# Kernel optimization log

Measured on AMD Instinct MI355X. Metric: run time of the kernel, lower is better.

Reference implementation:

```python
import jax, jax.numpy as jnp
import numpy as np
from math import factorial, sqrt

# ---- config: irreps_in1 = 128x0e+128x1o+128x2e, irreps_in2 = 1x0e+1x1o+1x2e, out = in1
MUL1, MUL2 = 128, 1
LS = [0, 1, 2]
DIMS = [2 * l + 1 for l in LS]
OFF1 = np.cumsum([0] + [MUL1 * d for d in DIMS])  # block offsets in x1 / out
OFF2 = np.cumsum([0] + [MUL2 * d for d in DIMS])  # block offsets in x2
# (i_in1, i_in2, i_out), all mode 'uvu', has_weight=True, path_weight=1
INSTR = [(0,0,0),(0,1,1),(0,2,2),(1,0,1),(1,1,0),(1,1,2),(1,2,1),(2,0,2),(2,1,1),(2,2,0),(2,2,2)]


def su2_cg(j1, m1, j2, m2, j3, m3):
    # SU(2) Clebsch-Gordan coefficient <j1 m1 j2 m2 | j3 m3> (e3nn convention)
    if m3 != m1 + m2:
        return 0.0
    f = factorial
    vmin = max(-j1 + j2 + m3, -j1 + m1, 0)
    vmax = min(j2 + j3 + m1, j3 - j1 + j2, j3 + m3)
    C = sqrt((2 * j3 + 1) * f(j3 + j1 - j2) * f(j3 - j1 + j2) * f(j1 + j2 - j3)
             * f(j3 + m3) * f(j3 - m3)
             / (f(j1 + j2 + j3 + 1) * f(j1 - m1) * f(j1 + m1) * f(j2 - m2) * f(j2 + m2)))
    S = 0.0
    for v in range(vmin, vmax + 1):
        S += (-1) ** (v + j2 + m2) * f(j2 + j3 + m1 - v) * f(j1 - m1 + v) \
             / (f(v) * f(j3 - j1 + j2 - v) * f(j3 + m3 - v) * f(v + j1 - j2 - m3))
    return C * S


def q_real_to_complex(l):
    # change of basis real SH -> complex SH (e3nn convention incl. (-i)^l phase)
    q = np.zeros((2 * l + 1, 2 * l + 1), dtype=np.complex128)
    for m in range(-l, 0):
        q[l + m, l + abs(m)] = 1 / sqrt(2)
        q[l + m, l - abs(m)] = -1j / sqrt(2)
    q[l, l] = 1.0
    for m in range(1, l + 1):
        q[l + m, l + abs(m)] = (-1) ** m / sqrt(2)
        q[l + m, l - abs(m)] = 1j * (-1) ** m / sqrt(2)
    return (-1j) ** l * q


def wigner_3j(l1, l2, l3):
    # real-basis Wigner 3j (e3nn), Frobenius-normalized
    C = np.zeros((2 * l1 + 1, 2 * l2 + 1, 2 * l3 + 1))
    for m1 in range(-l1, l1 + 1):
        for m2 in range(-l2, l2 + 1):
            for m3 in range(-l3, l3 + 1):
                C[l1 + m1, l2 + m2, l3 + m3] = su2_cg(l1, m1, l2, m2, l3, m3)
    Q1, Q2, Q3 = q_real_to_complex(l1), q_real_to_complex(l2), q_real_to_complex(l3)
    C = np.einsum('ij,kl,mn,ikn->jlm', Q1, Q2, np.conj(Q3.T), C.astype(np.complex128))
    C = np.real(C)
    return (C / np.linalg.norm(C)).astype(np.float32)


_N_PATHS_TO = np.zeros(len(LS), dtype=np.int64)
for _i1, _i2, _io in INSTR:
    _N_PATHS_TO[_io] += 1  # num_elements(uvu)=mul2=1, vars=1 -> element norm divisor


def setup_inputs() -> dict:
    key = jax.random.key(0)
    k1, k2, k3 = jax.random.split(key, 3)
    Z = 50000
    return {
        'x1': jax.random.normal(k1, (Z, int(OFF1[-1])), dtype=jnp.float32),
        'x2': jax.random.normal(k2, (Z, int(OFF2[-1])), dtype=jnp.float32),
        'weight': jax.random.normal(k3, (len(INSTR) * MUL1 * MUL2,), dtype=jnp.float32),
    }


def reference(x1, x2, weight):
    Z = x1.shape[0]
    outs = [jnp.zeros((Z, MUL1, DIMS[i]), x1.dtype) for i in range(len(LS))]
    woff = 0
    for (i1, i2, io) in INSTR:
        d1, d2, do = DIMS[i1], DIMS[i2], DIMS[io]
        x1b = x1[:, OFF1[i1]:OFF1[i1 + 1]].reshape(Z, MUL1, d1)
        x2b = x2[:, OFF2[i2]:OFF2[i2 + 1]].reshape(Z, MUL2, d2)
        w = weight[woff:woff + MUL1 * MUL2].reshape(MUL1, MUL2)
        woff += MUL1 * MUL2
        cg = jnp.asarray(wigner_3j(LS[i1], LS[i2], LS[io]))
        alpha = sqrt(do / float(_N_PATHS_TO[io]))  # component/element normalization
        outs[io] = outs[io] + alpha * jnp.einsum('ijk,uv,zui,zvj->zuk', cg, w, x1b, x2b)
    return jnp.concatenate([o.reshape(Z, -1) for o in outs], axis=1)
```

## Files before the change

### kernel.cpp

```cpp
#include <hip/hip_runtime.h>
#include <cmath>
#include <complex>
#include <algorithm>


namespace {

constexpr int NPATH = 11;
constexpr int P_I1[NPATH] = {0,0,0,1,1,1,1,2,2,2,2};
constexpr int P_I2[NPATH] = {0,1,2,0,1,1,2,0,1,2,2};
constexpr int P_IO[NPATH] = {0,1,2,1,0,2,1,2,1,0,2};
constexpr int DIM_[3]  = {1,3,5};
constexpr int LOFF[3]  = {0,1,4};
constexpr int P_OFF[NPATH] = {0,1,10,35,44,53,98,143,168,213,238};
constexpr int CG_TOTAL = 363;
constexpr int ROWF = 1152;
constexpr int ROWV = ROWF / 4;

typedef float v4f __attribute__((ext_vector_type(4)));

struct CGPack { float c[CG_TOTAL]; };


double fct(int n){ double r = 1.0; for(int i = 2; i <= n; ++i) r *= i; return r; }

double su2_cg(int j1,int m1,int j2,int m2,int j3,int m3){
  if (m3 != m1 + m2) return 0.0;
  int vmin = std::max(std::max(-j1 + j2 + m3, -j1 + m1), 0);
  int vmax = std::min(std::min(j2 + j3 + m1, j3 - j1 + j2), j3 + m3);
  double C = std::sqrt((2.0*j3 + 1.0) * fct(j3 + j1 - j2) * fct(j3 - j1 + j2) * fct(j1 + j2 - j3)
                       * fct(j3 + m3) * fct(j3 - m3)
                       / (fct(j1 + j2 + j3 + 1) * fct(j1 - m1) * fct(j1 + m1)
                          * fct(j2 - m2) * fct(j2 + m2)));
  double S = 0.0;
  for (int v = vmin; v <= vmax; ++v){
    double t = fct(j2 + j3 + m1 - v) * fct(j1 - m1 + v)
             / (fct(v) * fct(j3 - j1 + j2 - v) * fct(j3 + m3 - v) * fct(v + j1 - j2 - m3));
    S += (((v + j2 + m2) & 1) ? -1.0 : 1.0) * t;
  }
  return C * S;
}

void q_mat(int l, std::complex<double> q[5][5]){
  for (int a = 0; a < 5; ++a) for (int b = 0; b < 5; ++b) q[a][b] = 0.0;
  const double s = 1.0 / std::sqrt(2.0);
  for (int m = -l; m < 0; ++m){
    q[l+m][l-m] = s;
    q[l+m][l+m] = std::complex<double>(0.0, -s);
  }
  q[l][l] = 1.0;
  for (int m = 1; m <= l; ++m){
    double sg = (m & 1) ? -1.0 : 1.0;
    q[l+m][l+m] = sg * s;
    q[l+m][l-m] = std::complex<double>(0.0, sg * s);
  }
  std::complex<double> ph(1.0, 0.0);
  const std::complex<double> mi(0.0, -1.0);
  for (int t = 0; t < l; ++t) ph *= mi;
  for (int a = 0; a < 5; ++a) for (int b = 0; b < 5; ++b) q[a][b] *= ph;
}

void wigner3j(int l1, int l2, int l3, double scale, float* dst){
  const int n1 = 2*l1+1, n2 = 2*l2+1, n3 = 2*l3+1;
  std::complex<double> C[5][5][5];
  for (int a = 0; a < 5; ++a) for (int b = 0; b < 5; ++b) for (int c = 0; c < 5; ++c)
    C[a][b][c] = 0.0;
  for (int m1 = -l1; m1 <= l1; ++m1)
    for (int m2 = -l2; m2 <= l2; ++m2)
      for (int m3 = -l3; m3 <= l3; ++m3)
        C[l1+m1][l2+m2][l3+m3] = su2_cg(l1, m1, l2, m2, l3, m3);
  std::complex<double> Q1[5][5], Q2[5][5], Q3[5][5];
  q_mat(l1, Q1); q_mat(l2, Q2); q_mat(l3, Q3);
  double R[5][5][5];
  double nrm = 0.0;
  for (int a = 0; a < n1; ++a)
    for (int b = 0; b < n2; ++b)
      for (int c = 0; c < n3; ++c){
        std::complex<double> s(0.0, 0.0);
        for (int i = 0; i < n1; ++i)
          for (int k = 0; k < n2; ++k)
            for (int n = 0; n < n3; ++n)
              s += Q1[i][a] * Q2[k][b] * std::conj(Q3[n][c]) * C[i][k][n];
        R[a][b][c] = s.real();
        nrm += s.real() * s.real();
      }
  nrm = std::sqrt(nrm);
  for (int a = 0; a < n1; ++a)
    for (int b = 0; b < n2; ++b)
      for (int c = 0; c < n3; ++c)
        dst[(a*n2 + b)*n3 + c] = (float)(scale * R[a][b][c] / nrm);
}

CGPack build_pack(){
  CGPack p;
  int npaths_to[3] = {0,0,0};
  for (int i = 0; i < NPATH; ++i) npaths_to[P_IO[i]]++;
  for (int i = 0; i < NPATH; ++i){
    double alpha = std::sqrt((double)DIM_[P_IO[i]] / (double)npaths_to[P_IO[i]]);
    wigner3j(P_I1[i], P_I2[i], P_IO[i], alpha, p.c + P_OFF[i]);
  }
  return p;
}

}


__global__ __launch_bounds__(256) void tp_uvu_kernel(
    const float* __restrict__ x1, const float* __restrict__ x2,
    const float* __restrict__ w, float* __restrict__ out,
    int Z, CGPack cg)
{
  const int tid  = threadIdx.x;
  const int u    = tid & 127;
  const int zloc = tid >> 7;
  const long zbase = (long)blockIdx.x * 2;
  const long z     = zbase + zloc;

  __shared__ float s_x1[2 * ROWF];
  __shared__ float s_o [2 * ROWF];
  __shared__ float s_x2[2][9];

  const int nvalid_v = (int)((Z - zbase >= 2 ? 2 : (Z - zbase)) * ROWV);
  {
    const v4f* g1 = (const v4f*)(x1 + zbase * ROWF);
    v4f* s1 = (v4f*)s_x1;
    #pragma unroll
    for (int it = 0; it < 3; ++it) {
      int i = tid + it * 256;
      if (i < nvalid_v) s1[i] = g1[i];
    }
  }
  if (z < Z && u < 9) s_x2[zloc][u] = x2[z * 9 + u];
  __syncthreads();

  const float* x1z = s_x1 + zloc * ROWF;
  float xv2[9];
  #pragma unroll
  for (int j = 0; j < 9; ++j) xv2[j] = s_x2[zloc][j];

  float in1[9];
  in1[0] = x1z[u];
  #pragma unroll
  for (int i = 0; i < 3; ++i) in1[1+i] = x1z[128 + u*3 + i];
  #pragma unroll
  for (int i = 0; i < 5; ++i) in1[4+i] = x1z[512 + u*5 + i];

  float o[9];
  #pragma unroll
  for (int k = 0; k < 9; ++k) o[k] = 0.0f;

  #pragma unroll
  for (int p = 0; p < NPATH; ++p){
    const float wv = w[p * 128 + u];
    const int l1 = P_I1[p], l2 = P_I2[p], lo = P_IO[p];
    const int d1 = DIM_[l1], d2 = DIM_[l2], dd = DIM_[lo];
    const int b1 = LOFF[l1], b2 = LOFF[l2], bo = LOFF[lo];
    #pragma unroll
    for (int i = 0; i < d1; ++i){
      #pragma unroll
      for (int j = 0; j < d2; ++j){
        const float t = wv * in1[b1 + i] * xv2[b2 + j];
        #pragma unroll
        for (int k = 0; k < dd; ++k)
          o[bo + k] = fmaf(t, cg.c[P_OFF[p] + (i*d2 + j)*dd + k], o[bo + k]);
      }
    }
  }

  {
    float* oz = s_o + zloc * ROWF;
    oz[u] = o[0];
    #pragma unroll
    for (int k = 0; k < 3; ++k) oz[128 + u*3 + k] = o[1+k];
    #pragma unroll
    for (int k = 0; k < 5; ++k) oz[512 + u*5 + k] = o[4+k];
  }
  __syncthreads();
  {
    v4f* g_o = (v4f*)(out + zbase * ROWF);
    const v4f* s1 = (const v4f*)s_o;
    #pragma unroll
    for (int it = 0; it < 3; ++it) {
      int i = tid + it * 256;
      if (i < nvalid_v) __builtin_nontemporal_store(s1[i], &g_o[i]);
    }
  }
}

extern "C" void kernel_launch(void* const* d_in, const int* in_sizes, int n_in,
                              void* d_out, int out_size, void* d_ws, size_t ws_size,
                              hipStream_t stream)
{
  const float* x1 = (const float*)d_in[0];
  const float* x2 = (const float*)d_in[1];
  const float* w  = (const float*)d_in[2];
  float* out = (float*)d_out;
  const int Z = in_sizes[0] / ROWF;

  CGPack pack = build_pack();

  const int zpb = 2;
  dim3 grid((Z + zpb - 1) / zpb), block(128 * zpb);
  hipLaunchKernelGGL(tp_uvu_kernel, grid, block, 0, stream,
                     x1, x2, w, out, Z, pack);
}
```

Baseline: 396.3 us.

## Compute CG coefficients at compile time and skip zero terms in kernel

Moves the Wigner-3j/Clebsch-Gordan table construction into constexpr evaluation, so the coefficients become compile-time constants inside the kernel instead of a by-value kernel argument. With known values, the unrolled path loop can drop FMAs whose coefficient is zero, which removes most of the dense 363-term work. The per-path weight loads are also hoisted ahead of the compute loop. The risks are small numerical differences from the constexpr sqrt and the near-zero clamping. Host-side table building and the large kernel argument are removed as well.

```diff
diff --git a/kernel.cpp b/kernel.cpp
--- a/kernel.cpp
+++ b/kernel.cpp
@@ -1,6 +1,4 @@
 #include <hip/hip_runtime.h>
-#include <cmath>
-#include <complex>
 #include <algorithm>
 
 
@@ -22,85 +20,106 @@
 struct CGPack { float c[CG_TOTAL]; };
 
 
-double fct(int n){ double r = 1.0; for(int i = 2; i <= n; ++i) r *= i; return r; }
-
-double su2_cg(int j1,int m1,int j2,int m2,int j3,int m3){
+constexpr double cfct(int n){ double r = 1.0; for (int i = 2; i <= n; ++i) r *= i; return r; }
+
+constexpr double csqrt(double x){
+  if (x <= 0.0) return 0.0;
+  double g = x > 1.0 ? x : 1.0;
+  for (int i = 0; i < 64; ++i) g = 0.5 * (g + x / g);
+  return g;
+}
+
+struct cplx { double re = 0.0, im = 0.0; };
+constexpr cplx cmul(cplx a, cplx b){ return {a.re*b.re - a.im*b.im, a.re*b.im + a.im*b.re}; }
+constexpr cplx cconj(cplx a){ return {a.re, -a.im}; }
+
+constexpr double su2_cg(int j1,int m1,int j2,int m2,int j3,int m3){
   if (m3 != m1 + m2) return 0.0;
   int vmin = std::max(std::max(-j1 + j2 + m3, -j1 + m1), 0);
   int vmax = std::min(std::min(j2 + j3 + m1, j3 - j1 + j2), j3 + m3);
-  double C = std::sqrt((2.0*j3 + 1.0) * fct(j3 + j1 - j2) * fct(j3 - j1 + j2) * fct(j1 + j2 - j3)
-                       * fct(j3 + m3) * fct(j3 - m3)
-                       / (fct(j1 + j2 + j3 + 1) * fct(j1 - m1) * fct(j1 + m1)
-                          * fct(j2 - m2) * fct(j2 + m2)));
+  double C = csqrt((2.0*j3 + 1.0) * cfct(j3 + j1 - j2) * cfct(j3 - j1 + j2) * cfct(j1 + j2 - j3)
+                   * cfct(j3 + m3) * cfct(j3 - m3)
+                   / (cfct(j1 + j2 + j3 + 1) * cfct(j1 - m1) * cfct(j1 + m1)
+                      * cfct(j2 - m2) * cfct(j2 + m2)));
   double S = 0.0;
   for (int v = vmin; v <= vmax; ++v){
-    double t = fct(j2 + j3 + m1 - v) * fct(j1 - m1 + v)
-             / (fct(v) * fct(j3 - j1 + j2 - v) * fct(j3 + m3 - v) * fct(v + j1 - j2 - m3));
+    double t = cfct(j2 + j3 + m1 - v) * cfct(j1 - m1 + v)
+             / (cfct(v) * cfct(j3 - j1 + j2 - v) * cfct(j3 + m3 - v) * cfct(v + j1 - j2 - m3));
     S += (((v + j2 + m2) & 1) ? -1.0 : 1.0) * t;
   }
   return C * S;
 }
 
-void q_mat(int l, std::complex<double> q[5][5]){
-  for (int a = 0; a < 5; ++a) for (int b = 0; b < 5; ++b) q[a][b] = 0.0;
-  const double s = 1.0 / std::sqrt(2.0);
+struct QM { cplx q[5][5]; };
+
+constexpr QM q_mat(int l){
+  QM Q{};
+  const double s = 1.0 / csqrt(2.0);
   for (int m = -l; m < 0; ++m){
-    q[l+m][l-m] = s;
-    q[l+m][l+m] = std::complex<double>(0.0, -s);
-  }
-  q[l][l] = 1.0;
+    Q.q[l+m][l-m] = {s, 0.0};
+    Q.q[l+m][l+m] = {0.0, -s};
+  }
+  Q.q[l][l] = {1.0, 0.0};
   for (int m = 1; m <= l; ++m){
     double sg = (m & 1) ? -1.0 : 1.0;
-    q[l+m][l+m] = sg * s;
-    q[l+m][l-m] = std::complex<double>(0.0, sg * s);
-  }
-  std::complex<double> ph(1.0, 0.0);
-  const std::complex<double> mi(0.0, -1.0);
-  for (int t = 0; t < l; ++t) ph *= mi;
-  for (int a = 0; a < 5; ++a) for (int b = 0; b < 5; ++b) q[a][b] *= ph;
-}
-
-void wigner3j(int l1, int l2, int l3, double scale, float* dst){
+    Q.q[l+m][l+m] = {sg * s, 0.0};
+    Q.q[l+m][l-m] = {0.0, sg * s};
+  }
+  cplx ph{1.0, 0.0};
+  for (int t = 0; t < l; ++t) ph = cmul(ph, {0.0, -1.0});
+  for (int a = 0; a < 5; ++a) for (int b = 0; b < 5; ++b) Q.q[a][b] = cmul(Q.q[a][b], ph);
+  return Q;
+}
+
+constexpr void wigner3j(int l1, int l2, int l3, double scale, float* dst){
   const int n1 = 2*l1+1, n2 = 2*l2+1, n3 = 2*l3+1;
-  std::complex<double> C[5][5][5];
-  for (int a = 0; a < 5; ++a) for (int b = 0; b < 5; ++b) for (int c = 0; c < 5; ++c)
-    C[a][b][c] = 0.0;
-  for (int m1 = -l1; m1 <= l1; ++m1)
-    for (int m2 = -l2; m2 <= l2; ++m2)
-      for (int m3 = -l3; m3 <= l3; ++m3)
-        C[l1+m1][l2+m2][l3+m3] = su2_cg(l1, m1, l2, m2, l3, m3);
-  std::complex<double> Q1[5][5], Q2[5][5], Q3[5][5];
-  q_mat(l1, Q1); q_mat(l2, Q2); q_mat(l3, Q3);
-  double R[5][5][5];
+  const QM Q1 = q_mat(l1), Q2 = q_mat(l2), Q3 = q_mat(l3);
+  double R[5][5][5] = {};
   double nrm = 0.0;
+  for (int a = 0; a < n1; ++a){
+    const int il[2] = {a, n1 - 1 - a}; const int ic = (il[0] == il[1]) ? 1 : 2;
+    for (int b = 0; b < n2; ++b){
+      const int kl[2] = {b, n2 - 1 - b}; const int kc = (kl[0] == kl[1]) ? 1 : 2;
+      for (int c = 0; c < n3; ++c){
+        const int nl[2] = {c, n3 - 1 - c}; const int nc = (nl[0] == nl[1]) ? 1 : 2;
+        cplx s{0.0, 0.0};
+        for (int ii = 0; ii < ic; ++ii)
+          for (int kk = 0; kk < kc; ++kk)
+            for (int nn = 0; nn < nc; ++nn){
+              const int i = il[ii], k = kl[kk], n = nl[nn];
+              const double cg = su2_cg(l1, i - l1, l2, k - l2, l3, n - l3);
+              if (cg == 0.0) continue;
+              cplx t = cmul(Q1.q[i][a], Q2.q[k][b]);
+              t = cmul(t, cconj(Q3.q[n][c]));
+              s.re += t.re * cg; s.im += t.im * cg;
+            }
+        R[a][b][c] = s.re;
+        nrm += s.re * s.re;
+      }
+    }
+  }
+  nrm = csqrt(nrm);
   for (int a = 0; a < n1; ++a)
     for (int b = 0; b < n2; ++b)
       for (int c = 0; c < n3; ++c){
-        std::complex<double> s(0.0, 0.0);
-        for (int i = 0; i < n1; ++i)
-          for (int k = 0; k < n2; ++k)
-            for (int n = 0; n < n3; ++n)
-              s += Q1[i][a] * Q2[k][b] * std::conj(Q3[n][c]) * C[i][k][n];
-        R[a][b][c] = s.real();
-        nrm += s.real() * s.real();
+        double v = scale * R[a][b][c] / nrm;
+        if (v < 1e-10 && v > -1e-10) v = 0.0;
+        dst[(a*n2 + b)*n3 + c] = (float)v;
       }
-  nrm = std::sqrt(nrm);
-  for (int a = 0; a < n1; ++a)
-    for (int b = 0; b < n2; ++b)
-      for (int c = 0; c < n3; ++c)
-        dst[(a*n2 + b)*n3 + c] = (float)(scale * R[a][b][c] / nrm);
-}
-
-CGPack build_pack(){
-  CGPack p;
+}
+
+constexpr CGPack build_pack(){
+  CGPack p{};
   int npaths_to[3] = {0,0,0};
   for (int i = 0; i < NPATH; ++i) npaths_to[P_IO[i]]++;
   for (int i = 0; i < NPATH; ++i){
-    double alpha = std::sqrt((double)DIM_[P_IO[i]] / (double)npaths_to[P_IO[i]]);
+    double alpha = csqrt((double)DIM_[P_IO[i]] / (double)npaths_to[P_IO[i]]);
     wigner3j(P_I1[i], P_I2[i], P_IO[i], alpha, p.c + P_OFF[i]);
   }
   return p;
 }
+
+constexpr CGPack CG = build_pack();
 
 }
 
@@ -108,7 +127,7 @@
 __global__ __launch_bounds__(256) void tp_uvu_kernel(
     const float* __restrict__ x1, const float* __restrict__ x2,
     const float* __restrict__ w, float* __restrict__ out,
-    int Z, CGPack cg)
+    int Z)
 {
   const int tid  = threadIdx.x;
   const int u    = tid & 127;
@@ -138,6 +157,10 @@
   #pragma unroll
   for (int j = 0; j < 9; ++j) xv2[j] = s_x2[zloc][j];
 
+  float wvv[NPATH];
+  #pragma unroll
+  for (int p = 0; p < NPATH; ++p) wvv[p] = w[p * 128 + u];
+
   float in1[9];
   in1[0] = x1z[u];
   #pragma unroll
@@ -151,7 +174,7 @@
 
   #pragma unroll
   for (int p = 0; p < NPATH; ++p){
-    const float wv = w[p * 128 + u];
+    const float wv = wvv[p];
     const int l1 = P_I1[p], l2 = P_I2[p], lo = P_IO[p];
     const int d1 = DIM_[l1], d2 = DIM_[l2], dd = DIM_[lo];
     const int b1 = LOFF[l1], b2 = LOFF[l2], bo = LOFF[lo];
@@ -161,8 +184,11 @@
       for (int j = 0; j < d2; ++j){
         const float t = wv * in1[b1 + i] * xv2[b2 + j];
         #pragma unroll
-        for (int k = 0; k < dd; ++k)
-          o[bo + k] = fmaf(t, cg.c[P_OFF[p] + (i*d2 + j)*dd + k], o[bo + k]);
+        for (int k = 0; k < dd; ++k){
+          const float cgv = CG.c[P_OFF[p] + (i*d2 + j)*dd + k];
+          if (cgv != 0.0f)
+            o[bo + k] = fmaf(t, cgv, o[bo + k]);
+        }
       }
     }
   }
@@ -197,10 +223,8 @@
   float* out = (float*)d_out;
   const int Z = in_sizes[0] / ROWF;
 
-  CGPack pack = build_pack();
-
   const int zpb = 2;
   dim3 grid((Z + zpb - 1) / zpb), block(128 * zpb);
   hipLaunchKernelGGL(tp_uvu_kernel, grid, block, 0, stream,
-                     x1, x2, w, out, Z, pack);
-}
+                     x1, x2, w, out, Z);
+}
```

Measured after the change: 383.9 us. -3.2%, faster.
